# Kernel tuning notes

Measured on AMD Instinct MI355X. Metric: run time of the kernel, lower is better.

The kernel has to match this reference:

```python
import jax, jax.numpy as jnp
import numpy as np

N = 50000        # num nodes (num_paths)
E = 1_600_000    # num edges (avg degree 32)
W = 64           # window_size -> x feature dim
H = 128          # hidden_dimension
TEMP = 1.0       # temperature


def setup_inputs() -> dict:
    key = jax.random.key(0)
    k = jax.random.split(key, 6)
    x = jax.random.normal(k[0], (N, W), dtype=jnp.float32)
    y = jax.random.normal(k[1], (N,), dtype=jnp.float32)
    edge_index = jax.random.randint(k[2], (2, E), 0, N, dtype=jnp.int32)
    w1 = jax.random.normal(k[3], (2 * W, H), dtype=jnp.float32) / np.sqrt(2 * W)
    b1 = jnp.zeros((H,), dtype=jnp.float32)
    w2 = jax.random.normal(k[4], (H, 1), dtype=jnp.float32) / np.sqrt(H)
    b2 = jnp.zeros((1,), dtype=jnp.float32)
    return {"x": x, "y": y, "edge_index": edge_index,
            "w1": w1, "b1": b1, "w2": w2, "b2": b2}


def reference(x, y, edge_index, w1, b1, w2, b2):
    src, dst = edge_index[0], edge_index[1]
    # edge-wise gather + concat: [E, 2W]
    feat = jnp.concatenate([x[src], x[dst]], axis=1)
    # attention MLP: Linear -> ReLU -> Linear
    h = jax.nn.relu(feat @ w1 + b1)          # [E, H]
    logits = (h @ w2 + b2)[:, 0] / TEMP      # [E]
    # segment softmax over destination nodes (numerically stable)
    m = jax.ops.segment_max(logits, dst, num_segments=N)      # [N]
    e = jnp.exp(logits - m[dst])                               # [E]
    denom = jax.ops.segment_sum(e, dst, num_segments=N)       # [N]
    alpha = e / denom[dst]                                     # [E]
    # weighted scatter-sum aggregation
    y_hat = jax.ops.segment_sum(y[src] * alpha, dst, num_segments=N)  # [N]
    return y_hat, alpha[:, None]
```

## Files before the change

### kernel.cpp

```cpp
#include <hip/hip_runtime.h>
#include <hip/hip_bf16.h>

#define QSCALE 44.0f

__device__ __forceinline__ unsigned short f2bf(float f) {
    unsigned u = __float_as_uint(f);
    unsigned r = (u + 0x7fffu + ((u >> 16) & 1u)) >> 16;
    return (unsigned short)r;
}
__device__ __forceinline__ float bfu(unsigned short s) {
    return __uint_as_float(((unsigned)s) << 16);
}

__device__ __forceinline__ float dot8_relu_i8(const uint2 a, const uint2 b, const float* w2r) {
    float acc = 0.f;
#pragma unroll
    for (int i = 0; i < 4; ++i) {
        int va = (int)(char)(a.x >> (8 * i));
        int vb = (int)(char)(b.x >> (8 * i));
        acc += w2r[i] * (float)max(va + vb, 0);
    }
#pragma unroll
    for (int i = 0; i < 4; ++i) {
        int va = (int)(char)(a.y >> (8 * i));
        int vb = (int)(char)(b.y >> (8 * i));
        acc += w2r[4 + i] * (float)max(va + vb, 0);
    }
    return acc;
}

__global__ __launch_bounds__(256) void proj_kernel(
    const float* __restrict__ x, const float* __restrict__ w1, const float* __restrict__ b1,
    unsigned char* __restrict__ P, unsigned long long* __restrict__ agg, int N)
{
    __shared__ unsigned short wl[64 * 256];
    __shared__ float xs[32 * 64];
    const int t = threadIdx.x;
    const int n0 = blockIdx.x * 32;

    if (t < 32) {
        int n = n0 + t;
        if (n < N) agg[n] = 0ull;
    }

    for (int i = t; i < 64 * 256; i += 256) {
        int k = i >> 8, j = i & 255;
        float w = (j < 128) ? w1[k * 128 + j] : w1[(64 + k) * 128 + (j - 128)];
        wl[i] = f2bf(w);
    }
    for (int i = t; i < 32 * 64; i += 256) {
        int n = n0 + (i >> 6);
        xs[i] = (n < N) ? x[(size_t)n * 64 + (i & 63)] : 0.f;
    }
    __syncthreads();

    const int jg = t & 63;
    const int ng = t >> 6;
    const int j0 = jg * 4;

    float acc[8][4];
#pragma unroll
    for (int i = 0; i < 8; ++i)
#pragma unroll
        for (int c = 0; c < 4; ++c) acc[i][c] = 0.f;

    for (int k = 0; k < 64; k += 4) {
        float wv[4][4];
#pragma unroll
        for (int kk = 0; kk < 4; ++kk) {
            ushort4 wu = *(const ushort4*)&wl[(k + kk) * 256 + j0];
            wv[kk][0] = bfu(wu.x); wv[kk][1] = bfu(wu.y);
            wv[kk][2] = bfu(wu.z); wv[kk][3] = bfu(wu.w);
        }
#pragma unroll
        for (int i = 0; i < 8; ++i) {
            const float4 xv = *(const float4*)&xs[(ng * 8 + i) * 64 + k];
#pragma unroll
            for (int c = 0; c < 4; ++c)
                acc[i][c] += xv.x * wv[0][c] + xv.y * wv[1][c] + xv.z * wv[2][c] + xv.w * wv[3][c];
        }
    }

    float bb[4] = {0.f, 0.f, 0.f, 0.f};
    if (j0 < 128) {
#pragma unroll
        for (int c = 0; c < 4; ++c) bb[c] = b1[j0 + c];
    }

#pragma unroll
    for (int i = 0; i < 8; ++i) {
        int n = n0 + ng * 8 + i;
        if (n < N) {
            unsigned pk = 0;
#pragma unroll
            for (int c = 0; c < 4; ++c) {
                float v = (acc[i][c] + bb[c]) * QSCALE;
                int q = __float2int_rn(fminf(fmaxf(v, -127.f), 127.f));
                pk |= ((unsigned)(q & 0xff)) << (8 * c);
            }
            *(unsigned*)(P + (size_t)n * 256 + j0) = pk;
        }
    }
}

__global__ __launch_bounds__(256) void edge_logit_kernel(
    const unsigned char* __restrict__ P, const int* __restrict__ ei,
    const float* __restrict__ y,
    const float* __restrict__ w2, const float* __restrict__ b2,
    float* __restrict__ elog, unsigned long long* __restrict__ agg, int E)
{
    const int lane = threadIdx.x & 15;
    float w2r[8];
#pragma unroll
    for (int c = 0; c < 8; ++c) w2r[c] = w2[lane * 8 + c] * (1.0f / QSCALE);
    const float b2s = b2[0];

    const int slot = (blockIdx.x * 256 + threadIdx.x) >> 4;
    const int nslots = (gridDim.x * 256) >> 4;

    for (int e = slot; e < E; e += nslots) {
        const int s = ei[e];
        const int d = ei[E + e];
        const uint2 a = *(const uint2*)(P + (size_t)s * 256 + lane * 8);
        const uint2 b = *(const uint2*)(P + (size_t)d * 256 + 128 + lane * 8);

        float acc = dot8_relu_i8(a, b, w2r);
        acc += __shfl_xor(acc, 1);
        acc += __shfl_xor(acc, 2);
        acc += __shfl_xor(acc, 4);
        acc += __shfl_xor(acc, 8);

        if (lane == 0) {
            float ev = __expf(acc + b2s);
            elog[e] = ev;
            float flo = fminf(ev * 65536.f, 1.0e9f);
            float fhi = fmaxf(fminf(y[s] * ev * 16384.f, 1.0e9f), -1.0e9f);
            unsigned int qlo = (unsigned int)__float2int_rn(flo);
            int          qhi = __float2int_rn(fhi);
            unsigned long long packed =
                ((unsigned long long)(unsigned int)qhi << 32) | (unsigned long long)qlo;
            atomicAdd(&agg[d], packed);
        }
    }
}

__global__ void node_decode_kernel(const unsigned long long* __restrict__ agg,
                                   float* __restrict__ inv_d,
                                   float* __restrict__ yhat, int N) {
    int i = blockIdx.x * 256 + threadIdx.x;
    if (i >= N) return;
    unsigned long long v = agg[i];
    unsigned int lo = (unsigned int)(v & 0xffffffffull);
    int          hi = (int)(v >> 32);
    if (lo != 0u) {
        float flo = (float)lo;
        yhat[i]  = 4.0f * (float)hi / flo;
        inv_d[i] = 65536.0f / flo;
    } else {
        yhat[i]  = 0.f;
        inv_d[i] = 0.f;
    }
}

__global__ __launch_bounds__(256) void alpha_norm_kernel(
    const int* __restrict__ ei, float* __restrict__ elog,
    const float* __restrict__ inv_d, int E)
{
    int e = blockIdx.x * 256 + threadIdx.x;
    if (e >= E) return;
    int d = ei[E + e];
    elog[e] = elog[e] * inv_d[d];
}

extern "C" void kernel_launch(void* const* d_in, const int* in_sizes, int n_in,
                              void* d_out, int out_size, void* d_ws, size_t ws_size,
                              hipStream_t stream) {
    const float* x  = (const float*)d_in[0];
    const float* y  = (const float*)d_in[1];
    const int*   ei = (const int*)d_in[2];
    const float* w1 = (const float*)d_in[3];
    const float* b1 = (const float*)d_in[4];
    const float* w2 = (const float*)d_in[5];
    const float* b2 = (const float*)d_in[6];

    const int N = in_sizes[1];
    const int E = in_sizes[2] / 2;

    float* out  = (float*)d_out;
    float* yhat = out;
    float* elog = out + N;

    char* ws = (char*)d_ws;
    unsigned char* P = (unsigned char*)ws;
    size_t Pbytes = (size_t)N * 256;
    unsigned long long* agg = (unsigned long long*)(ws + Pbytes);
    float* inv_d = (float*)(ws + Pbytes + (size_t)N * 8);

    proj_kernel<<<(N + 31) / 32, 256, 0, stream>>>(x, w1, b1, P, agg, N);
    edge_logit_kernel<<<2048, 256, 0, stream>>>(P, ei, y, w2, b2, elog, agg, E);
    node_decode_kernel<<<(N + 255) / 256, 256, 0, stream>>>(agg, inv_d, yhat, N);
    alpha_norm_kernel<<<(E + 255) / 256, 256, 0, stream>>>(ei, elog, inv_d, E);
}
```

Before: 214.8 us.

## Persist proj blocks over node tiles and use 8 lanes per edge

The projection kernel becomes a grid-stride persistent kernel with 512 blocks. Each block converts the W1 weights to bf16 in shared memory once, instead of once per 32-node tile, which cuts redundant weight loads and conversions. The edge kernel now gives each edge 8 lanes with 16-byte loads instead of 16 lanes with 8-byte loads. This halves the shuffle reduction depth and doubles the edges processed per wavefront, at the cost of more registers per thread.

```diff
diff --git a/kernel.cpp b/kernel.cpp
--- a/kernel.cpp
+++ b/kernel.cpp
@@ -12,19 +12,13 @@
     return __uint_as_float(((unsigned)s) << 16);
 }
 
-__device__ __forceinline__ float dot8_relu_i8(const uint2 a, const uint2 b, const float* w2r) {
+__device__ __forceinline__ float dot4_i8(unsigned ax, unsigned bx, const float* w) {
     float acc = 0.f;
 #pragma unroll
     for (int i = 0; i < 4; ++i) {
-        int va = (int)(char)(a.x >> (8 * i));
-        int vb = (int)(char)(b.x >> (8 * i));
-        acc += w2r[i] * (float)max(va + vb, 0);
-    }
-#pragma unroll
-    for (int i = 0; i < 4; ++i) {
-        int va = (int)(char)(a.y >> (8 * i));
-        int vb = (int)(char)(b.y >> (8 * i));
-        acc += w2r[4 + i] * (float)max(va + vb, 0);
+        int va = (int)(char)(ax >> (8 * i));
+        int vb = (int)(char)(bx >> (8 * i));
+        acc += w[i] * (float)max(va + vb, 0);
     }
     return acc;
 }
@@ -36,69 +30,74 @@
     __shared__ unsigned short wl[64 * 256];
     __shared__ float xs[32 * 64];
     const int t = threadIdx.x;
-    const int n0 = blockIdx.x * 32;
-
-    if (t < 32) {
-        int n = n0 + t;
-        if (n < N) agg[n] = 0ull;
-    }
 
     for (int i = t; i < 64 * 256; i += 256) {
         int k = i >> 8, j = i & 255;
         float w = (j < 128) ? w1[k * 128 + j] : w1[(64 + k) * 128 + (j - 128)];
         wl[i] = f2bf(w);
     }
-    for (int i = t; i < 32 * 64; i += 256) {
-        int n = n0 + (i >> 6);
-        xs[i] = (n < N) ? x[(size_t)n * 64 + (i & 63)] : 0.f;
-    }
-    __syncthreads();
 
     const int jg = t & 63;
     const int ng = t >> 6;
     const int j0 = jg * 4;
 
-    float acc[8][4];
-#pragma unroll
-    for (int i = 0; i < 8; ++i)
-#pragma unroll
-        for (int c = 0; c < 4; ++c) acc[i][c] = 0.f;
-
-    for (int k = 0; k < 64; k += 4) {
-        float wv[4][4];
-#pragma unroll
-        for (int kk = 0; kk < 4; ++kk) {
-            ushort4 wu = *(const ushort4*)&wl[(k + kk) * 256 + j0];
-            wv[kk][0] = bfu(wu.x); wv[kk][1] = bfu(wu.y);
-            wv[kk][2] = bfu(wu.z); wv[kk][3] = bfu(wu.w);
-        }
-#pragma unroll
-        for (int i = 0; i < 8; ++i) {
-            const float4 xv = *(const float4*)&xs[(ng * 8 + i) * 64 + k];
-#pragma unroll
-            for (int c = 0; c < 4; ++c)
-                acc[i][c] += xv.x * wv[0][c] + xv.y * wv[1][c] + xv.z * wv[2][c] + xv.w * wv[3][c];
-        }
-    }
-
     float bb[4] = {0.f, 0.f, 0.f, 0.f};
     if (j0 < 128) {
 #pragma unroll
         for (int c = 0; c < 4; ++c) bb[c] = b1[j0 + c];
     }
 
-#pragma unroll
-    for (int i = 0; i < 8; ++i) {
-        int n = n0 + ng * 8 + i;
-        if (n < N) {
-            unsigned pk = 0;
-#pragma unroll
-            for (int c = 0; c < 4; ++c) {
-                float v = (acc[i][c] + bb[c]) * QSCALE;
-                int q = __float2int_rn(fminf(fmaxf(v, -127.f), 127.f));
-                pk |= ((unsigned)(q & 0xff)) << (8 * c);
+    const int ntiles = (N + 31) / 32;
+    for (int tile = blockIdx.x; tile < ntiles; tile += gridDim.x) {
+        const int n0 = tile * 32;
+
+        __syncthreads();
+        if (t < 32) {
+            int n = n0 + t;
+            if (n < N) agg[n] = 0ull;
+        }
+        for (int i = t; i < 32 * 64; i += 256) {
+            int n = n0 + (i >> 6);
+            xs[i] = (n < N) ? x[(size_t)n * 64 + (i & 63)] : 0.f;
+        }
+        __syncthreads();
+
+        float acc[8][4];
+#pragma unroll
+        for (int i = 0; i < 8; ++i)
+#pragma unroll
+            for (int c = 0; c < 4; ++c) acc[i][c] = 0.f;
+
+        for (int k = 0; k < 64; k += 4) {
+            float wv[4][4];
+#pragma unroll
+            for (int kk = 0; kk < 4; ++kk) {
+                ushort4 wu = *(const ushort4*)&wl[(k + kk) * 256 + j0];
+                wv[kk][0] = bfu(wu.x); wv[kk][1] = bfu(wu.y);
+                wv[kk][2] = bfu(wu.z); wv[kk][3] = bfu(wu.w);
             }
-            *(unsigned*)(P + (size_t)n * 256 + j0) = pk;
+#pragma unroll
+            for (int i = 0; i < 8; ++i) {
+                const float4 xv = *(const float4*)&xs[(ng * 8 + i) * 64 + k];
+#pragma unroll
+                for (int c = 0; c < 4; ++c)
+                    acc[i][c] += xv.x * wv[0][c] + xv.y * wv[1][c] + xv.z * wv[2][c] + xv.w * wv[3][c];
+            }
+        }
+
+#pragma unroll
+        for (int i = 0; i < 8; ++i) {
+            int n = n0 + ng * 8 + i;
+            if (n < N) {
+                unsigned pk = 0;
+#pragma unroll
+                for (int c = 0; c < 4; ++c) {
+                    float v = (acc[i][c] + bb[c]) * QSCALE;
+                    int q = __float2int_rn(fminf(fmaxf(v, -127.f), 127.f));
+                    pk |= ((unsigned)(q & 0xff)) << (8 * c);
+                }
+                *(unsigned*)(P + (size_t)n * 256 + j0) = pk;
+            }
         }
     }
 }
@@ -109,26 +108,30 @@
     const float* __restrict__ w2, const float* __restrict__ b2,
     float* __restrict__ elog, unsigned long long* __restrict__ agg, int E)
 {
-    const int lane = threadIdx.x & 15;
-    float w2r[8];
-#pragma unroll
-    for (int c = 0; c < 8; ++c) w2r[c] = w2[lane * 8 + c] * (1.0f / QSCALE);
+    const int lane = threadIdx.x & 7;
+    float w2r[16];
+#pragma unroll
+    for (int c = 0; c < 16; ++c) w2r[c] = w2[lane * 16 + c] * (1.0f / QSCALE);
     const float b2s = b2[0];
 
-    const int slot = (blockIdx.x * 256 + threadIdx.x) >> 4;
-    const int nslots = (gridDim.x * 256) >> 4;
+    const int slot = (blockIdx.x * 256 + threadIdx.x) >> 3;
+    const int nslots = (gridDim.x * 256) >> 3;
 
     for (int e = slot; e < E; e += nslots) {
         const int s = ei[e];
         const int d = ei[E + e];
-        const uint2 a = *(const uint2*)(P + (size_t)s * 256 + lane * 8);
-        const uint2 b = *(const uint2*)(P + (size_t)d * 256 + 128 + lane * 8);
-
-        float acc = dot8_relu_i8(a, b, w2r);
+        const uint4 a = *(const uint4*)(P + (size_t)s * 256 + lane * 16);
+        const uint4 b = *(const uint4*)(P + (size_t)d * 256 + 128 + lane * 16);
+
+        float acc;
+        acc  = dot4_i8(a.x, b.x, w2r + 0);
+        acc += dot4_i8(a.y, b.y, w2r + 4);
+        acc += dot4_i8(a.z, b.z, w2r + 8);
+        acc += dot4_i8(a.w, b.w, w2r + 12);
+
         acc += __shfl_xor(acc, 1);
         acc += __shfl_xor(acc, 2);
         acc += __shfl_xor(acc, 4);
-        acc += __shfl_xor(acc, 8);
 
         if (lane == 0) {
             float ev = __expf(acc + b2s);
@@ -196,7 +199,7 @@
     unsigned long long* agg = (unsigned long long*)(ws + Pbytes);
     float* inv_d = (float*)(ws + Pbytes + (size_t)N * 8);
 
-    proj_kernel<<<(N + 31) / 32, 256, 0, stream>>>(x, w1, b1, P, agg, N);
+    proj_kernel<<<512, 256, 0, stream>>>(x, w1, b1, P, agg, N);
     edge_logit_kernel<<<2048, 256, 0, stream>>>(P, ei, y, w2, b2, elog, agg, E);
     node_decode_kernel<<<(N + 255) / 256, 256, 0, stream>>>(agg, inv_d, yhat, N);
     alpha_norm_kernel<<<(E + 255) / 256, 256, 0, stream>>>(ei, elog, inv_d, E);
```

Measured after the change: 210.8 us. No clear change (-1.8%).
